# Kernel optimization log

Hardware: AMD Instinct MI355X
Metric: run time of the kernel (lower is better)

The kernel has to match this reference:

```python
import jax, jax.numpy as jnp
import numpy as np

BLOCK_SIZE = 32
STRIDE = 16
DIM = 128


def setup_inputs() -> dict:
    key = jax.random.key(0)
    ks = jax.random.split(key, 6)
    B, N, C = 8, 16384, DIM
    x = jax.random.normal(ks[0], (B, N, C), dtype=jnp.float32)
    pos = jax.random.normal(ks[1], (1, BLOCK_SIZE, C), dtype=jnp.float32) * 0.02
    # torch Linear stores W:(out,in); we store transposed (in,out) for x @ W
    fan_in1 = C * BLOCK_SIZE
    W1 = jax.random.uniform(ks[2], (fan_in1, 2 * C), dtype=jnp.float32,
                            minval=-1.0, maxval=1.0) / jnp.sqrt(fan_in1)
    b1 = jax.random.uniform(ks[3], (2 * C,), dtype=jnp.float32,
                            minval=-1.0, maxval=1.0) / jnp.sqrt(fan_in1)
    fan_in2 = 2 * C
    W2 = jax.random.uniform(ks[4], (fan_in2, C), dtype=jnp.float32,
                            minval=-1.0, maxval=1.0) / jnp.sqrt(fan_in2)
    b2 = jax.random.uniform(ks[5], (C,), dtype=jnp.float32,
                            minval=-1.0, maxval=1.0) / jnp.sqrt(fan_in2)
    return {"x": x, "pos": pos, "W1": W1, "b1": b1, "W2": W2, "b2": b2}


def reference(x, pos, W1, b1, W2, b2):
    B, N, C = x.shape
    l, d = BLOCK_SIZE, STRIDE
    if N < l:  # static shapes -> plain Python branch is fine
        return jnp.mean(x, axis=1, keepdims=True)
    num_blocks = (N - l) // d + 1
    # overlapping sliding-window gather: (nb, l) token indices
    idx = jnp.arange(num_blocks)[:, None] * d + jnp.arange(l)[None, :]
    blocks = x[:, idx, :] + pos[None]            # (B, nb, l, C)
    blocks = blocks.reshape(B, num_blocks, l * C)  # (B, nb, l*C)
    h = jax.nn.gelu(blocks @ W1 + b1, approximate=False)  # exact erf GELU (torch default)
    return h @ W2 + b2                           # (B, nb, C)
```

## Files before the change

kernel.cpp:

```cpp
#include <hip/hip_runtime.h>
#include <hip/hip_bf16.h>
#include <math.h>


typedef __attribute__((ext_vector_type(8))) short short8;
typedef __attribute__((ext_vector_type(4))) float f4;

#define OFF_BT   0u
#define OFF_W2T  (2u << 20)
#define OFF_PART ((2u << 20) + (64u << 10))
#define OFF_BIAS ((2u << 20) + (128u << 10))
#define OFF_P    (4u << 20)

static __device__ __forceinline__ unsigned short f2bf(float f) {
  union { float f; unsigned u; } v; v.f = f;
  return (unsigned short)((v.u + 0x7FFFu + ((v.u >> 16) & 1u)) >> 16);
}
static __device__ __forceinline__ float bf2f(unsigned short h) {
  union { unsigned u; float f; } v; v.u = ((unsigned)h) << 16;
  return v.f;
}
static __device__ __forceinline__ void gload_lds16(const void* g, void* l) {
  __builtin_amdgcn_global_load_lds(
      (const __attribute__((address_space(1))) void*)g,
      (__attribute__((address_space(3))) void*)l, 16, 0, 0);
}

__global__ __launch_bounds__(256) void k_prep(const float* __restrict__ W1,
                                              const float* __restrict__ pos,
                                              const float* __restrict__ W2,
                                              unsigned short* __restrict__ Bt,
                                              unsigned short* __restrict__ W2t,
                                              float* __restrict__ part) {
  __shared__ float T[64][65];
  const int w = blockIdx.x;
  const int t = threadIdx.x;
  if (w >= 256) {
    const int n = w - 256;
    W2t[n * 256 + t] = f2bf(W2[t * 128 + n]);
    return;
  }
  const int h = w >> 7, rem = w & 127, kt = rem >> 2, nt = rem & 3;
  const int krow0 = h * 2048 + kt * 64, col0 = nt * 64;
  const int lr = t >> 2, lc = (t & 3) * 16;
  const float* src = W1 + (size_t)(krow0 + lr) * 256 + col0 + lc;
#pragma unroll
  for (int i = 0; i < 4; ++i) {
    f4 v = *(const f4*)(src + i * 4);
#pragma unroll
    for (int q = 0; q < 4; ++q) T[lr][lc + i * 4 + q] = v[q];
  }
  __syncthreads();
  if (t < 64) {
    float s = 0.f;
#pragma unroll 8
    for (int k = 0; k < 64; ++k) s += T[k][t] * pos[krow0 + k];
    part[(h * 32 + kt) * 256 + col0 + t] = s;
  }
  const int nl = t >> 2, kc = (t & 3) * 16;
  short8 o0, o1;
#pragma unroll
  for (int i = 0; i < 8; ++i) o0[i] = (short)f2bf(T[kc + i][nl]);
#pragma unroll
  for (int i = 0; i < 8; ++i) o1[i] = (short)f2bf(T[kc + 8 + i][nl]);
  unsigned short* dst = Bt + (size_t)(256 * h + col0 + nl) * 2048 + kt * 64 + kc;
  *(short8*)dst = o0;
  *(short8*)(dst + 8) = o1;
}

__global__ __launch_bounds__(256) void k_bias(const float* __restrict__ b1,
                                              const float* __restrict__ part,
                                              float* __restrict__ bias) {
  int n = threadIdx.x;
  float s = b1[n];
#pragma unroll 8
  for (int g = 0; g < 64; ++g) s += part[g * 256 + n];
  bias[n] = s;
}

__global__ __launch_bounds__(256, 2) void k_gemm(const float* __restrict__ X,
                                                 const unsigned short* __restrict__ Bt,
                                                 unsigned short* __restrict__ P) {
  __shared__ __align__(16) char lds[2][24576];
  const int orig = blockIdx.x;
  const int wg = (orig & 7) * 64 + (orig >> 3);
  const int mt = wg >> 3;
  const int nt = (wg >> 1) & 3;
  const int ksp = wg & 1;
  const int m0 = mt * 128, n0 = nt * 128, k0 = ksp * 1024;
  const int t = threadIdx.x;
  const int wid = t >> 6, lane = t & 63;
  const int wm = (wid >> 1) * 64, wn = (wid & 1) * 64;

  f4 acc[4][4];
#pragma unroll
  for (int i = 0; i < 4; ++i)
#pragma unroll
    for (int j = 0; j < 4; ++j) acc[i][j] = f4{0.f, 0.f, 0.f, 0.f};

#define ISSUE(BUF, KT)                                                     \
  do {                                                                     \
    const int kf = k0 + (KT) * 32;                                         \
    _Pragma("unroll") for (int ii = 0; ii < 4; ++ii) {                     \
      const int s = ii * 256 + t;                                          \
      const int row = s >> 3, c8 = s & 7;                                  \
      gload_lds16(X + (size_t)(m0 + row) * 2048 + kf +                     \
                      ((c8 ^ (row & 7)) << 2),                             \
                  &lds[BUF][ii * 4096 + wid * 1024]);                      \
    }                                                                      \
    _Pragma("unroll") for (int ii = 0; ii < 2; ++ii) {                     \
      const int s = ii * 256 + t;                                          \
      const int row = s >> 2, c4 = s & 3;                                  \
      gload_lds16(Bt + (size_t)(n0 + row) * 2048 + kf +                    \
                      ((c4 ^ (row & 3)) << 3),                             \
                  &lds[BUF][16384 + ii * 4096 + wid * 1024]);              \
    }                                                                      \
  } while (0)

#define COMPUTE(BUF)                                                       \
  do {                                                                     \
    const float* Ab = (const float*)&lds[BUF][0];                          \
    const unsigned short* Bb = (const unsigned short*)&lds[BUF][16384];    \
    short8 af[4], bfv[4];                                                  \
    const int jk = lane >> 4;                                              \
    _Pragma("unroll") for (int m = 0; m < 4; ++m) {                        \
      const int row = wm + m * 16 + (lane & 15);                           \
      const int e = row & 7;                                               \
      f4 lo = *(const f4*)(Ab + row * 32 + (((2 * jk) ^ e) << 2));         \
      f4 hi = *(const f4*)(Ab + row * 32 + (((2 * jk + 1) ^ e) << 2));     \
      union { short8 s8; unsigned u[4]; } pk;                              \
      asm("v_cvt_pk_bf16_f32 %0, %1, %2" : "=v"(pk.u[0])                   \
          : "v"(lo[0]), "v"(lo[1]));                                       \
      asm("v_cvt_pk_bf16_f32 %0, %1, %2" : "=v"(pk.u[1])                   \
          : "v"(lo[2]), "v"(lo[3]));                                       \
      asm("v_cvt_pk_bf16_f32 %0, %1, %2" : "=v"(pk.u[2])                   \
          : "v"(hi[0]), "v"(hi[1]));                                       \
      asm("v_cvt_pk_bf16_f32 %0, %1, %2" : "=v"(pk.u[3])                   \
          : "v"(hi[2]), "v"(hi[3]));                                       \
      af[m] = pk.s8;                                                       \
    }                                                                      \
    _Pragma("unroll") for (int n = 0; n < 4; ++n) {                        \
      const int row = wn + n * 16 + (lane & 15);                           \
      bfv[n] = *(const short8*)(Bb + row * 32 +                            \
                                ((jk ^ (row & 3)) << 3));                  \
    }                                                                      \
    __builtin_amdgcn_s_setprio(1);                                         \
    _Pragma("unroll") for (int m = 0; m < 4; ++m)                          \
      _Pragma("unroll") for (int n = 0; n < 4; ++n)                        \
        acc[m][n] = __builtin_amdgcn_mfma_f32_16x16x32_bf16(               \
            af[m], bfv[n], acc[m][n], 0, 0, 0);                            \
    __builtin_amdgcn_s_setprio(0);                                         \
  } while (0)

  ISSUE(0, 0);
  ISSUE(1, 1);
  __builtin_amdgcn_sched_barrier(0);
  asm volatile("s_waitcnt vmcnt(6)" ::: "memory");
  __builtin_amdgcn_s_barrier();
  __builtin_amdgcn_sched_barrier(0);

#pragma unroll 2
  for (int kt = 0; kt < 32; ++kt) {
    COMPUTE(kt & 1);
    __builtin_amdgcn_sched_barrier(0);
    __builtin_amdgcn_s_barrier();
    __builtin_amdgcn_sched_barrier(0);
    if (kt < 30) {
      ISSUE(kt & 1, kt + 2);
      __builtin_amdgcn_sched_barrier(0);
      asm volatile("s_waitcnt vmcnt(6)" ::: "memory");
      __builtin_amdgcn_s_barrier();
      __builtin_amdgcn_sched_barrier(0);
    } else if (kt == 30) {
      asm volatile("s_waitcnt vmcnt(0)" ::: "memory");
      __builtin_amdgcn_s_barrier();
      __builtin_amdgcn_sched_barrier(0);
    }
  }
#undef ISSUE
#undef COMPUTE

  unsigned short* Pp = P + (size_t)ksp * (8192 * 512);
  const int mb = m0 + wm, nb = n0 + wn;
#pragma unroll
  for (int m = 0; m < 4; ++m)
#pragma unroll
    for (int n = 0; n < 4; ++n) {
      const int row0 = mb + m * 16 + ((lane >> 4) << 2);
      const int col = nb + n * 16 + (lane & 15);
#pragma unroll
      for (int r = 0; r < 4; ++r)
        Pp[(size_t)(row0 + r) * 512 + col] = f2bf(acc[m][n][r]);
    }
}

__global__ __launch_bounds__(256) void k_comb(const unsigned short* __restrict__ P,
                                              const unsigned short* __restrict__ W2t,
                                              const float* __restrict__ bias,
                                              const float* __restrict__ b2,
                                              float* __restrict__ out) {
  __shared__ unsigned short W2s[128 * 256];
  __shared__ unsigned short Hs[32 * 256];
  const unsigned short* Pa = P;
  const unsigned short* Pb = P + (size_t)8192 * 512;
  const int wg = blockIdx.x;
  const int b = wg >> 5, jt = wg & 31;
  const int j0 = jt * 32;
  const int t = threadIdx.x;

  {
    const int row = t >> 1, halfc = (t & 1) * 128;
    const unsigned short* src = W2t + row * 256 + halfc;
    const int cbw = halfc >> 3;
#pragma unroll
    for (int i = 0; i < 16; ++i) {
      short8 v = *(const short8*)(src + i * 8);
      const int c = (cbw + i) ^ (row & 7);
      *(short8*)&W2s[row * 256 + c * 8] = v;
    }
  }
  {
    const int r = t >> 3, seg = t & 7;
    const int j = j0 + r;
    const size_t m = (size_t)b * 1024 + j;
    const size_t mp1 = (j < 1023) ? m + 1 : m;
    const unsigned short* p0a = Pa + m * 512 + seg * 32;
    const unsigned short* p0b = Pb + m * 512 + seg * 32;
    const unsigned short* p1a = Pa + mp1 * 512 + 256 + seg * 32;
    const unsigned short* p1b = Pb + mp1 * 512 + 256 + seg * 32;
    const float* bs = bias + seg * 32;
    const int cbh = seg * 4;
#pragma unroll
    for (int i = 0; i < 4; ++i) {
      short8 v0a = *(const short8*)(p0a + i * 8);
      short8 v0b = *(const short8*)(p0b + i * 8);
      short8 v1a = *(const short8*)(p1a + i * 8);
      short8 v1b = *(const short8*)(p1b + i * 8);
      short8 pk;
#pragma unroll
      for (int q = 0; q < 8; ++q) {
        float f = bf2f((unsigned short)v0a[q]) + bf2f((unsigned short)v0b[q]) +
                  bf2f((unsigned short)v1a[q]) + bf2f((unsigned short)v1b[q]) +
                  bs[i * 8 + q];
        float g = 0.5f * f * (1.f + erff(f * 0.70710678118f));
        pk[q] = (short)f2bf(g);
      }
      const int c = (cbh + i) ^ (r & 7);
      *(short8*)&Hs[r * 256 + c * 8] = pk;
    }
  }
  __syncthreads();

  const int wid = t >> 6, lane = t & 63;
  f4 acc[2][2];
#pragma unroll
  for (int i = 0; i < 2; ++i)
#pragma unroll
    for (int j = 0; j < 2; ++j) acc[i][j] = f4{0.f, 0.f, 0.f, 0.f};

#pragma unroll
  for (int ks = 0; ks < 8; ++ks) {
    short8 af[2], bfr[2];
    const int cc = ks * 4 + (lane >> 4);
#pragma unroll
    for (int f = 0; f < 2; ++f) {
      const int ra = f * 16 + (lane & 15);
      af[f] = *(const short8*)&Hs[ra * 256 + ((cc ^ (ra & 7)) << 3)];
      const int rb = wid * 32 + f * 16 + (lane & 15);
      bfr[f] = *(const short8*)&W2s[rb * 256 + ((cc ^ (rb & 7)) << 3)];
    }
#pragma unroll
    for (int i = 0; i < 2; ++i)
#pragma unroll
      for (int j = 0; j < 2; ++j)
        acc[i][j] = __builtin_amdgcn_mfma_f32_16x16x32_bf16(af[i], bfr[j],
                                                            acc[i][j], 0, 0, 0);
  }
#pragma unroll
  for (int i = 0; i < 2; ++i)
#pragma unroll
    for (int j = 0; j < 2; ++j) {
      const int row0 = i * 16 + ((lane >> 4) << 2);
      const int col = wid * 32 + j * 16 + (lane & 15);
      const float bb = b2[col];
#pragma unroll
      for (int r = 0; r < 4; ++r) {
        const int jj = j0 + row0 + r;
        if (jj < 1023)
          out[((size_t)b * 1023 + jj) * 128 + col] = acc[i][j][r] + bb;
      }
    }
}

extern "C" void kernel_launch(void* const* d_in, const int* in_sizes, int n_in,
                              void* d_out, int out_size, void* d_ws, size_t ws_size,
                              hipStream_t stream) {
  const float* x   = (const float*)d_in[0];
  const float* pos = (const float*)d_in[1];
  const float* W1  = (const float*)d_in[2];
  const float* b1  = (const float*)d_in[3];
  const float* W2  = (const float*)d_in[4];
  const float* b2  = (const float*)d_in[5];
  float* out = (float*)d_out;
  char* ws = (char*)d_ws;
  unsigned short* Bt  = (unsigned short*)(ws + OFF_BT);
  unsigned short* W2t = (unsigned short*)(ws + OFF_W2T);
  float* part         = (float*)(ws + OFF_PART);
  float* bias         = (float*)(ws + OFF_BIAS);
  unsigned short* P   = (unsigned short*)(ws + OFF_P);

  k_prep<<<384, 256, 0, stream>>>(W1, pos, W2, Bt, W2t, part);
  k_bias<<<1, 256, 0, stream>>>(b1, part, bias);
  k_gemm<<<512, 256, 0, stream>>>(x, Bt, P);
  k_comb<<<256, 256, 0, stream>>>(P, W2t, bias, b2, out);
}
```

Before: 54.14 us.

## Enlarge GEMM tiles to 256x256 with four-way split-K and 512-thread blocks

The main GEMM moves from 128x128 tiles with a two-way K split over 512 blocks of 256 threads to 256x256 tiles with a four-way K split over 256 blocks of 512 threads. Each wave now computes a 64x128 output using 32 accumulators. The larger tiles raise operand reuse from LDS and cut global reloads of X and Bt. The combine kernel now sums four bf16 partial buffers instead of two, which doubles the partial-sum traffic and workspace. Register pressure rises, and with 256 blocks the machine gets about one block per CU, so occupancy and latency hiding may suffer.

After: 58.62 us. +8.3%, slower.

```diff
diff --git a/kernel.cpp b/kernel.cpp
--- a/kernel.cpp
+++ b/kernel.cpp
@@ -78,56 +78,56 @@
   bias[n] = s;
 }
 
-__global__ __launch_bounds__(256, 2) void k_gemm(const float* __restrict__ X,
-                                                 const unsigned short* __restrict__ Bt,
-                                                 unsigned short* __restrict__ P) {
-  __shared__ __align__(16) char lds[2][24576];
+__global__ __launch_bounds__(512) void k_gemm(const float* __restrict__ X,
+                                              const unsigned short* __restrict__ Bt,
+                                              unsigned short* __restrict__ P) {
+  __shared__ __align__(16) char lds[2][49152];
   const int orig = blockIdx.x;
-  const int wg = (orig & 7) * 64 + (orig >> 3);
+  const int wg = (orig & 7) * 32 + (orig >> 3);
   const int mt = wg >> 3;
-  const int nt = (wg >> 1) & 3;
-  const int ksp = wg & 1;
-  const int m0 = mt * 128, n0 = nt * 128, k0 = ksp * 1024;
+  const int nt = (wg >> 2) & 1;
+  const int ksp = wg & 3;
+  const int m0 = mt * 256, n0 = nt * 256, k0 = ksp * 512;
   const int t = threadIdx.x;
   const int wid = t >> 6, lane = t & 63;
-  const int wm = (wid >> 1) * 64, wn = (wid & 1) * 64;
-
-  f4 acc[4][4];
-#pragma unroll
-  for (int i = 0; i < 4; ++i)
-#pragma unroll
-    for (int j = 0; j < 4; ++j) acc[i][j] = f4{0.f, 0.f, 0.f, 0.f};
+  const int wr = wid >> 1, wc = wid & 1;
+
+  f4 acc[4][8];
+#pragma unroll
+  for (int m = 0; m < 4; ++m)
+#pragma unroll
+    for (int n = 0; n < 8; ++n) acc[m][n] = f4{0.f, 0.f, 0.f, 0.f};
 
 #define ISSUE(BUF, KT)                                                     \
   do {                                                                     \
     const int kf = k0 + (KT) * 32;                                         \
     _Pragma("unroll") for (int ii = 0; ii < 4; ++ii) {                     \
-      const int s = ii * 256 + t;                                          \
+      const int s = ii * 512 + t;                                          \
       const int row = s >> 3, c8 = s & 7;                                  \
       gload_lds16(X + (size_t)(m0 + row) * 2048 + kf +                     \
                       ((c8 ^ (row & 7)) << 2),                             \
-                  &lds[BUF][ii * 4096 + wid * 1024]);                      \
+                  &lds[BUF][ii * 8192 + wid * 1024]);                      \
     }                                                                      \
     _Pragma("unroll") for (int ii = 0; ii < 2; ++ii) {                     \
-      const int s = ii * 256 + t;                                          \
+      const int s = ii * 512 + t;                                          \
       const int row = s >> 2, c4 = s & 3;                                  \
       gload_lds16(Bt + (size_t)(n0 + row) * 2048 + kf +                    \
                       ((c4 ^ (row & 3)) << 3),                             \
-                  &lds[BUF][16384 + ii * 4096 + wid * 1024]);              \
+                  &lds[BUF][32768 + ii * 8192 + wid * 1024]);              \
     }                                                                      \
   } while (0)
 
 #define COMPUTE(BUF)                                                       \
   do {                                                                     \
     const float* Ab = (const float*)&lds[BUF][0];                          \
-    const unsigned short* Bb = (const unsigned short*)&lds[BUF][16384];    \
-    short8 af[4], bfv[4];                                                  \
-    const int jk = lane >> 4;                                              \
+    const unsigned short* Bb = (const unsigned short*)&lds[BUF][32768];    \
+    short8 af[4], bfv[8];                                                  \
+    const int q = lane >> 4;                                               \
     _Pragma("unroll") for (int m = 0; m < 4; ++m) {                        \
-      const int row = wm + m * 16 + (lane & 15);                           \
+      const int row = wr * 64 + m * 16 + (lane & 15);                      \
       const int e = row & 7;                                               \
-      f4 lo = *(const f4*)(Ab + row * 32 + (((2 * jk) ^ e) << 2));         \
-      f4 hi = *(const f4*)(Ab + row * 32 + (((2 * jk + 1) ^ e) << 2));     \
+      f4 lo = *(const f4*)(Ab + row * 32 + (((2 * q) ^ e) << 2));          \
+      f4 hi = *(const f4*)(Ab + row * 32 + (((2 * q + 1) ^ e) << 2));      \
       union { short8 s8; unsigned u[4]; } pk;                              \
       asm("v_cvt_pk_bf16_f32 %0, %1, %2" : "=v"(pk.u[0])                   \
           : "v"(lo[0]), "v"(lo[1]));                                       \
@@ -139,14 +139,14 @@
           : "v"(hi[2]), "v"(hi[3]));                                       \
       af[m] = pk.s8;                                                       \
     }                                                                      \
-    _Pragma("unroll") for (int n = 0; n < 4; ++n) {                        \
-      const int row = wn + n * 16 + (lane & 15);                           \
-      bfv[n] = *(const short8*)(Bb + row * 32 +                            \
-                                ((jk ^ (row & 3)) << 3));                  \
+    _Pragma("unroll") for (int n = 0; n < 8; ++n) {                        \
+      const int row = wc * 128 + n * 16 + (lane & 15);                     \
+      bfv[n] = *(const short8*)((const unsigned short*)Bb + row * 32 +     \
+                                ((q ^ (row & 3)) << 3));                   \
     }                                                                      \
     __builtin_amdgcn_s_setprio(1);                                         \
     _Pragma("unroll") for (int m = 0; m < 4; ++m)                          \
-      _Pragma("unroll") for (int n = 0; n < 4; ++n)                        \
+      _Pragma("unroll") for (int n = 0; n < 8; ++n)                        \
         acc[m][n] = __builtin_amdgcn_mfma_f32_16x16x32_bf16(               \
             af[m], bfv[n], acc[m][n], 0, 0, 0);                            \
     __builtin_amdgcn_s_setprio(0);                                         \
@@ -160,18 +160,18 @@
   __builtin_amdgcn_sched_barrier(0);
 
 #pragma unroll 2
-  for (int kt = 0; kt < 32; ++kt) {
+  for (int kt = 0; kt < 16; ++kt) {
     COMPUTE(kt & 1);
     __builtin_amdgcn_sched_barrier(0);
     __builtin_amdgcn_s_barrier();
     __builtin_amdgcn_sched_barrier(0);
-    if (kt < 30) {
+    if (kt < 14) {
       ISSUE(kt & 1, kt + 2);
       __builtin_amdgcn_sched_barrier(0);
       asm volatile("s_waitcnt vmcnt(6)" ::: "memory");
       __builtin_amdgcn_s_barrier();
       __builtin_amdgcn_sched_barrier(0);
-    } else if (kt == 30) {
+    } else if (kt == 14) {
       asm volatile("s_waitcnt vmcnt(0)" ::: "memory");
       __builtin_amdgcn_s_barrier();
       __builtin_amdgcn_sched_barrier(0);
@@ -181,11 +181,11 @@
 #undef COMPUTE
 
   unsigned short* Pp = P + (size_t)ksp * (8192 * 512);
-  const int mb = m0 + wm, nb = n0 + wn;
+  const int mb = m0 + wr * 64, nb = n0 + wc * 128;
 #pragma unroll
   for (int m = 0; m < 4; ++m)
 #pragma unroll
-    for (int n = 0; n < 4; ++n) {
+    for (int n = 0; n < 8; ++n) {
       const int row0 = mb + m * 16 + ((lane >> 4) << 2);
       const int col = nb + n * 16 + (lane & 15);
 #pragma unroll
@@ -201,8 +201,6 @@
                                               float* __restrict__ out) {
   __shared__ unsigned short W2s[128 * 256];
   __shared__ unsigned short Hs[32 * 256];
-  const unsigned short* Pa = P;
-  const unsigned short* Pb = P + (size_t)8192 * 512;
   const int wg = blockIdx.x;
   const int b = wg >> 5, jt = wg & 31;
   const int j0 = jt * 32;
@@ -224,25 +222,26 @@
     const int j = j0 + r;
     const size_t m = (size_t)b * 1024 + j;
     const size_t mp1 = (j < 1023) ? m + 1 : m;
-    const unsigned short* p0a = Pa + m * 512 + seg * 32;
-    const unsigned short* p0b = Pb + m * 512 + seg * 32;
-    const unsigned short* p1a = Pa + mp1 * 512 + 256 + seg * 32;
-    const unsigned short* p1b = Pb + mp1 * 512 + 256 + seg * 32;
     const float* bs = bias + seg * 32;
     const int cbh = seg * 4;
 #pragma unroll
     for (int i = 0; i < 4; ++i) {
-      short8 v0a = *(const short8*)(p0a + i * 8);
-      short8 v0b = *(const short8*)(p0b + i * 8);
-      short8 v1a = *(const short8*)(p1a + i * 8);
-      short8 v1b = *(const short8*)(p1b + i * 8);
+      float f0[8];
+#pragma unroll
+      for (int q = 0; q < 8; ++q) f0[q] = bs[i * 8 + q];
+#pragma unroll
+      for (int ksp = 0; ksp < 4; ++ksp) {
+        const unsigned short* Pk = P + (size_t)ksp * (8192 * 512);
+        short8 v0 = *(const short8*)(Pk + m * 512 + seg * 32 + i * 8);
+        short8 v1 = *(const short8*)(Pk + mp1 * 512 + 256 + seg * 32 + i * 8);
+#pragma unroll
+        for (int q = 0; q < 8; ++q)
+          f0[q] += bf2f((unsigned short)v0[q]) + bf2f((unsigned short)v1[q]);
+      }
       short8 pk;
 #pragma unroll
       for (int q = 0; q < 8; ++q) {
-        float f = bf2f((unsigned short)v0a[q]) + bf2f((unsigned short)v0b[q]) +
-                  bf2f((unsigned short)v1a[q]) + bf2f((unsigned short)v1b[q]) +
-                  bs[i * 8 + q];
-        float g = 0.5f * f * (1.f + erff(f * 0.70710678118f));
+        float g = 0.5f * f0[q] * (1.f + erff(f0[q] * 0.70710678118f));
         pk[q] = (short)f2bf(g);
       }
       const int c = (cbh + i) ^ (r & 7);
@@ -311,6 +310,6 @@
 
   k_prep<<<384, 256, 0, stream>>>(W1, pos, W2, Bt, W2t, part);
   k_bias<<<1, 256, 0, stream>>>(b1, part, bias);
-  k_gemm<<<512, 256, 0, stream>>>(x, Bt, P);
+  k_gemm<<<256, 512, 0, stream>>>(x, Bt, P);
   k_comb<<<256, 256, 0, stream>>>(P, W2t, bias, b2, out);
 }
```
